# Optimization experiments

Measured on AMD Instinct MI355X. Metric: run time of the kernel, lower is better.

## Reference

```python
import jax, jax.numpy as jnp
import numpy as np

N, D = 8192, 128
TEMPERATURE = 0.5


def _l2_normalize(x, eps):
    # matches F.normalize / utils.sim_matrix norm clamping
    n = jnp.linalg.norm(x, axis=1, keepdims=True)
    return x / jnp.maximum(n, eps)


def setup_inputs() -> dict:
    key = jax.random.key(0)
    k1, k2, k3 = jax.random.split(key, 3)
    nodes = jax.random.normal(k1, (N, D), dtype=jnp.float32)
    pair_nodes = jax.random.normal(k2, (N, D), dtype=jnp.float32)
    nodes_labels = jax.random.randint(k3, (N,), 0, 20).astype(jnp.int64)
    # standard NT-Xent self-mask: exclude diagonal from the denominator
    mask = jnp.eye(N, dtype=bool)
    return {"nodes": nodes, "pair_nodes": pair_nodes,
            "nodes_labels": nodes_labels, "mask": mask}


def reference(nodes, pair_nodes, nodes_labels, mask):
    # z, z_p: F.normalize(..., dim=1), eps=1e-12
    z = _l2_normalize(nodes, 1e-12)
    z_p = _l2_normalize(pair_nodes, 1e-12)
    # pairwise cosine similarity [N, N] == z @ z_p.T since rows are unit-norm
    positive_similarity = jnp.einsum('id,jd->ij', z, z_p)
    nominator = jnp.exp(positive_similarity / TEMPERATURE)  # [N, N]
    # utils.sim_matrix(nodes, nodes): cosine sim matrix with eps=1e-8 clamp
    zn = _l2_normalize(nodes, 1e-8)
    similarity_matrix = jnp.einsum('id,jd->ij', zn, zn)  # [N, N]
    denominator = (~mask).astype(jnp.float32) * jnp.exp(similarity_matrix / TEMPERATURE)
    den_sum = jnp.sum(denominator, axis=1)  # [N]
    # torch broadcasting: [N,N] / [N] divides along the LAST axis (columns)
    loss_partial = -jnp.log(nominator / den_sum[None, :])
    loss = jnp.sum(loss_partial) / nodes.shape[0]
    return loss
```

## Files before the change

### kernel.cpp

```cpp
#include <hip/hip_runtime.h>

#define N 8192
#define D 128
#define NT 64
#define EXP_SCALE 2.8853900817779268f

typedef __bf16 bf16;
typedef __bf16 bf16x2 __attribute__((ext_vector_type(2)));
typedef __bf16 bf16x8 __attribute__((ext_vector_type(8)));
typedef float f32x4 __attribute__((ext_vector_type(4)));

#define ZBF_OFF 0
#define DEN_OFF (N * D * 2)
#define S_OFF   (DEN_OFF + N * 4)
#define SP_OFF  (S_OFF + 512)

__global__ __launch_bounds__(256) void norm_kernel(
    const float* __restrict__ nodes, const float* __restrict__ pair,
    bf16* __restrict__ zbf, float* __restrict__ svec, float* __restrict__ spvec)
{
    __shared__ float red[4][128];
    const int tid = threadIdx.x;
    const int lane = tid & 63, wave = tid >> 6;
    const bool isPair = blockIdx.x >= 128;
    const float* src = isPair ? pair : nodes;
    const int row0 = (blockIdx.x & 127) * 64 + wave * 16;

    float acc0 = 0.f, acc1 = 0.f;
    for (int rr = 0; rr < 16; ++rr) {
        const int row = row0 + rr;
        const float2 x = *(const float2*)(src + row * D + lane * 2);
        float ss = x.x * x.x + x.y * x.y;
        #pragma unroll
        for (int m = 32; m >= 1; m >>= 1) ss += __shfl_xor(ss, m, 64);
        const float nrm = sqrtf(ss);
        const float inv12 = 1.f / fmaxf(nrm, 1e-12f);
        acc0 += x.x * inv12;
        acc1 += x.y * inv12;
        if (!isPair) {
            const float inv8 = 1.f / fmaxf(nrm, 1e-8f);
            bf16x2 pk;
            pk[0] = (bf16)(x.x * inv8);
            pk[1] = (bf16)(x.y * inv8);
            *(bf16x2*)(zbf + row * D + lane * 2) = pk;
        }
    }
    red[wave][lane * 2]     = acc0;
    red[wave][lane * 2 + 1] = acc1;
    __syncthreads();
    if (tid < 128) {
        float* dst = isPair ? spvec : svec;
        atomicAdd(&dst[tid], red[0][tid] + red[1][tid] + red[2][tid] + red[3][tid]);
    }
}

#define LDP 80

__global__ __launch_bounds__(256) void gemm_kernel(
    const bf16* __restrict__ zbf, float* __restrict__ den)
{
    __shared__ bf16 As[128 * LDP];
    __shared__ bf16 Bs[128 * LDP];
    __shared__ float rowacc[128];
    __shared__ float colacc[128];

    int b = blockIdx.x;
    int ti = (int)((2.0 * NT + 1.0 - sqrt((2.0 * NT + 1.0) * (2.0 * NT + 1.0) - 8.0 * (double)b)) * 0.5);
    while (ti > 0 && ti * (2 * NT + 1 - ti) / 2 > b) --ti;
    while ((ti + 1) * (2 * NT - ti) / 2 <= b) ++ti;
    const int tj = ti + (b - ti * (2 * NT + 1 - ti) / 2);
    const bool diag = (ti == tj);

    const int tid  = threadIdx.x;
    const int lane = tid & 63, wave = tid >> 6;
    const int wm = wave >> 1, wn = wave & 1;
    const int quad = lane >> 4, c = lane & 15;
    const int ibase = ti * 128;
    const int jbase = tj * 128;

    if (tid < 128) { rowacc[tid] = 0.f; colacc[tid] = 0.f; }

    f32x4 acc[4][4];
    #pragma unroll
    for (int i = 0; i < 4; ++i)
        #pragma unroll
        for (int j = 0; j < 4; ++j) acc[i][j] = (f32x4){0.f, 0.f, 0.f, 0.f};

    #pragma unroll
    for (int kh = 0; kh < 2; ++kh) {
        __syncthreads();
        #pragma unroll
        for (int i = 0; i < 4; ++i) {
            const int chunk = tid + 256 * i;
            const int row = chunk >> 3;
            const int c8  = (chunk & 7) * 8;
            const uint4 va = *(const uint4*)(zbf + (ibase + row) * D + kh * 64 + c8);
            const uint4 vb = *(const uint4*)(zbf + (jbase + row) * D + kh * 64 + c8);
            *(uint4*)(&As[row * LDP + c8]) = va;
            *(uint4*)(&Bs[row * LDP + c8]) = vb;
        }
        __syncthreads();
        #pragma unroll
        for (int ks = 0; ks < 2; ++ks) {
            const int kk = ks * 32;
            bf16x8 af[4], bfr[4];
            #pragma unroll
            for (int mi = 0; mi < 4; ++mi)
                af[mi] = *(const bf16x8*)(&As[(wm * 64 + mi * 16 + c) * LDP + kk + quad * 8]);
            #pragma unroll
            for (int ni = 0; ni < 4; ++ni)
                bfr[ni] = *(const bf16x8*)(&Bs[(wn * 64 + ni * 16 + c) * LDP + kk + quad * 8]);
            #pragma unroll
            for (int mi = 0; mi < 4; ++mi)
                #pragma unroll
                for (int ni = 0; ni < 4; ++ni)
                    acc[mi][ni] = __builtin_amdgcn_mfma_f32_16x16x32_bf16(
                        af[mi], bfr[ni], acc[mi][ni], 0, 0, 0);
        }
    }

    float rowp[4][4];
    float colp[4];
    #pragma unroll
    for (int mi = 0; mi < 4; ++mi)
        #pragma unroll
        for (int r = 0; r < 4; ++r) rowp[mi][r] = 0.f;
    #pragma unroll
    for (int ni = 0; ni < 4; ++ni) colp[ni] = 0.f;

    #pragma unroll
    for (int mi = 0; mi < 4; ++mi) {
        const int lrow0 = wm * 64 + mi * 16 + quad * 4;
        #pragma unroll
        for (int ni = 0; ni < 4; ++ni) {
            const int lcol = wn * 64 + ni * 16 + c;
            const f32x4 cv = acc[mi][ni];
            #pragma unroll
            for (int r = 0; r < 4; ++r) {
                float e = __builtin_amdgcn_exp2f(cv[r] * EXP_SCALE);
                if (diag && (lrow0 + r == lcol)) e = 0.f;
                rowp[mi][r] += e;
                colp[ni]    += e;
            }
        }
    }

    #pragma unroll
    for (int mi = 0; mi < 4; ++mi)
        #pragma unroll
        for (int r = 0; r < 4; ++r) {
            #pragma unroll
            for (int m = 1; m <= 8; m <<= 1)
                rowp[mi][r] += __shfl_xor(rowp[mi][r], m, 64);
        }
    if (c == 0) {
        #pragma unroll
        for (int mi = 0; mi < 4; ++mi)
            #pragma unroll
            for (int r = 0; r < 4; ++r)
                atomicAdd(&rowacc[wm * 64 + mi * 16 + quad * 4 + r], rowp[mi][r]);
    }

    if (!diag) {
        #pragma unroll
        for (int ni = 0; ni < 4; ++ni) {
            colp[ni] += __shfl_xor(colp[ni], 16, 64);
            colp[ni] += __shfl_xor(colp[ni], 32, 64);
        }
        if (quad == 0) {
            #pragma unroll
            for (int ni = 0; ni < 4; ++ni)
                atomicAdd(&colacc[wn * 64 + ni * 16 + c], colp[ni]);
        }
    }

    __syncthreads();
    if (tid < 128) {
        atomicAdd(&den[ibase + tid], rowacc[tid]);
        if (!diag) atomicAdd(&den[jbase + tid], colacc[tid]);
    }
}

__global__ __launch_bounds__(256) void final_kernel(
    const float* __restrict__ den, const float* __restrict__ s,
    const float* __restrict__ sp, float* __restrict__ out)
{
    __shared__ float red[4];
    const int tid = threadIdx.x;
    float v = 0.f;
    for (int j = tid; j < N; j += 256) v += logf(den[j]);
    if (tid < 128) v -= s[tid] * sp[tid] * (1.f / 4096.f);
    #pragma unroll
    for (int m = 32; m >= 1; m >>= 1) v += __shfl_xor(v, m, 64);
    if ((tid & 63) == 0) red[tid >> 6] = v;
    __syncthreads();
    if (tid == 0) out[0] = red[0] + red[1] + red[2] + red[3];
}

extern "C" void kernel_launch(void* const* d_in, const int* in_sizes, int n_in,
                              void* d_out, int out_size, void* d_ws, size_t ws_size,
                              hipStream_t stream)
{
    const float* nodes = (const float*)d_in[0];
    const float* pair  = (const float*)d_in[1];

    char*  ws  = (char*)d_ws;
    bf16*  zbf = (bf16*)(ws + ZBF_OFF);
    float* den = (float*)(ws + DEN_OFF);
    float* s   = (float*)(ws + S_OFF);
    float* sp  = (float*)(ws + SP_OFF);

    hipMemsetAsync(ws + DEN_OFF, 0, N * 4 + 1024, stream);

    hipLaunchKernelGGL(norm_kernel, dim3(256), dim3(256), 0, stream,
                       nodes, pair, zbf, s, sp);
    hipLaunchKernelGGL(gemm_kernel, dim3(NT * (NT + 1) / 2), dim3(256), 0, stream,
                       zbf, den);
    hipLaunchKernelGGL(final_kernel, dim3(1), dim3(256), 0, stream,
                       den, s, sp, (float*)d_out);
}
```

Baseline: 352.8 us.

## Prescale normalized rows, widen norm kernel, prefetch second K-half into registers

The norm kernel now has 16 lanes handle each row with float4 loads, runs 1024 blocks, and writes the bf16 rows scaled by sqrt(2/ln2). This lets the GEMM epilogue call exp2 directly without a multiply. The GEMM kernel loads both K halves into registers up front and stores the second half to shared memory after the first half's MFMAs, so global-load latency overlaps compute. The prescaling shifts where bf16 rounding happens, so numerics change slightly, and holding the extra tile in registers raises register pressure.

Measured after the change: 361.7 us. +2.5%, slower.

```diff
diff --git a/kernel.cpp b/kernel.cpp
--- a/kernel.cpp
+++ b/kernel.cpp
@@ -3,10 +3,9 @@
 #define N 8192
 #define D 128
 #define NT 64
-#define EXP_SCALE 2.8853900817779268f
+#define PRESCALE 1.6986435984699773f
 
 typedef __bf16 bf16;
-typedef __bf16 bf16x2 __attribute__((ext_vector_type(2)));
 typedef __bf16 bf16x8 __attribute__((ext_vector_type(8)));
 typedef float f32x4 __attribute__((ext_vector_type(4)));
 
@@ -22,31 +21,42 @@
     __shared__ float red[4][128];
     const int tid = threadIdx.x;
     const int lane = tid & 63, wave = tid >> 6;
-    const bool isPair = blockIdx.x >= 128;
+    const int g = lane & 15, q = lane >> 4;
+    const bool isPair = blockIdx.x >= 512;
     const float* src = isPair ? pair : nodes;
-    const int row0 = (blockIdx.x & 127) * 64 + wave * 16;
-
-    float acc0 = 0.f, acc1 = 0.f;
-    for (int rr = 0; rr < 16; ++rr) {
-        const int row = row0 + rr;
-        const float2 x = *(const float2*)(src + row * D + lane * 2);
-        float ss = x.x * x.x + x.y * x.y;
-        #pragma unroll
-        for (int m = 32; m >= 1; m >>= 1) ss += __shfl_xor(ss, m, 64);
-        const float nrm = sqrtf(ss);
-        const float inv12 = 1.f / fmaxf(nrm, 1e-12f);
-        acc0 += x.x * inv12;
-        acc1 += x.y * inv12;
-        if (!isPair) {
-            const float inv8 = 1.f / fmaxf(nrm, 1e-8f);
-            bf16x2 pk;
-            pk[0] = (bf16)(x.x * inv8);
-            pk[1] = (bf16)(x.y * inv8);
-            *(bf16x2*)(zbf + row * D + lane * 2) = pk;
-        }
-    }
-    red[wave][lane * 2]     = acc0;
-    red[wave][lane * 2 + 1] = acc1;
+    const int row = (blockIdx.x & 511) * 16 + wave * 4 + q;
+
+    const float4 x0 = *(const float4*)(src + row * D + g * 8);
+    const float4 x1 = *(const float4*)(src + row * D + g * 8 + 4);
+    float ss = x0.x * x0.x + x0.y * x0.y + x0.z * x0.z + x0.w * x0.w
+             + x1.x * x1.x + x1.y * x1.y + x1.z * x1.z + x1.w * x1.w;
+    #pragma unroll
+    for (int m = 1; m <= 8; m <<= 1) ss += __shfl_xor(ss, m, 64);
+    const float nrm = sqrtf(ss);
+    const float inv12 = 1.f / fmaxf(nrm, 1e-12f);
+
+    float a[8] = { x0.x * inv12, x0.y * inv12, x0.z * inv12, x0.w * inv12,
+                   x1.x * inv12, x1.y * inv12, x1.z * inv12, x1.w * inv12 };
+
+    if (!isPair) {
+        const float sc = PRESCALE / fmaxf(nrm, 1e-8f);
+        bf16x8 pk;
+        pk[0] = (bf16)(x0.x * sc); pk[1] = (bf16)(x0.y * sc);
+        pk[2] = (bf16)(x0.z * sc); pk[3] = (bf16)(x0.w * sc);
+        pk[4] = (bf16)(x1.x * sc); pk[5] = (bf16)(x1.y * sc);
+        pk[6] = (bf16)(x1.z * sc); pk[7] = (bf16)(x1.w * sc);
+        *(bf16x8*)(zbf + row * D + g * 8) = pk;
+    }
+
+    #pragma unroll
+    for (int k = 0; k < 8; ++k) {
+        a[k] += __shfl_xor(a[k], 16, 64);
+        a[k] += __shfl_xor(a[k], 32, 64);
+    }
+    if (q == 0) {
+        #pragma unroll
+        for (int k = 0; k < 8; ++k) red[wave][g * 8 + k] = a[k];
+    }
     __syncthreads();
     if (tid < 128) {
         float* dst = isPair ? spvec : svec;
@@ -86,20 +96,32 @@
         #pragma unroll
         for (int j = 0; j < 4; ++j) acc[i][j] = (f32x4){0.f, 0.f, 0.f, 0.f};
 
+    uint4 va[4], vb[4];
+    #pragma unroll
+    for (int i = 0; i < 4; ++i) {
+        const int chunk = tid + 256 * i;
+        const int row = chunk >> 3, c8 = (chunk & 7) * 8;
+        va[i] = *(const uint4*)(zbf + (ibase + row) * D + c8);
+        vb[i] = *(const uint4*)(zbf + (jbase + row) * D + c8);
+    }
+    #pragma unroll
+    for (int i = 0; i < 4; ++i) {
+        const int chunk = tid + 256 * i;
+        const int row = chunk >> 3, c8 = (chunk & 7) * 8;
+        *(uint4*)(&As[row * LDP + c8]) = va[i];
+        *(uint4*)(&Bs[row * LDP + c8]) = vb[i];
+    }
+    #pragma unroll
+    for (int i = 0; i < 4; ++i) {
+        const int chunk = tid + 256 * i;
+        const int row = chunk >> 3, c8 = (chunk & 7) * 8;
+        va[i] = *(const uint4*)(zbf + (ibase + row) * D + 64 + c8);
+        vb[i] = *(const uint4*)(zbf + (jbase + row) * D + 64 + c8);
+    }
+    __syncthreads();
+
     #pragma unroll
     for (int kh = 0; kh < 2; ++kh) {
-        __syncthreads();
-        #pragma unroll
-        for (int i = 0; i < 4; ++i) {
-            const int chunk = tid + 256 * i;
-            const int row = chunk >> 3;
-            const int c8  = (chunk & 7) * 8;
-            const uint4 va = *(const uint4*)(zbf + (ibase + row) * D + kh * 64 + c8);
-            const uint4 vb = *(const uint4*)(zbf + (jbase + row) * D + kh * 64 + c8);
-            *(uint4*)(&As[row * LDP + c8]) = va;
-            *(uint4*)(&Bs[row * LDP + c8]) = vb;
-        }
-        __syncthreads();
         #pragma unroll
         for (int ks = 0; ks < 2; ++ks) {
             const int kk = ks * 32;
@@ -117,6 +139,17 @@
                     acc[mi][ni] = __builtin_amdgcn_mfma_f32_16x16x32_bf16(
                         af[mi], bfr[ni], acc[mi][ni], 0, 0, 0);
         }
+        if (kh == 0) {
+            __syncthreads();
+            #pragma unroll
+            for (int i = 0; i < 4; ++i) {
+                const int chunk = tid + 256 * i;
+                const int row = chunk >> 3, c8 = (chunk & 7) * 8;
+                *(uint4*)(&As[row * LDP + c8]) = va[i];
+                *(uint4*)(&Bs[row * LDP + c8]) = vb[i];
+            }
+            __syncthreads();
+        }
     }
 
     float rowp[4][4];
@@ -137,7 +170,7 @@
             const f32x4 cv = acc[mi][ni];
             #pragma unroll
             for (int r = 0; r < 4; ++r) {
-                float e = __builtin_amdgcn_exp2f(cv[r] * EXP_SCALE);
+                float e = __builtin_amdgcn_exp2f(cv[r]);
                 if (diag && (lrow0 + r == lcol)) e = 0.f;
                 rowp[mi][r] += e;
                 colp[ni]    += e;
@@ -212,7 +245,7 @@
 
     hipMemsetAsync(ws + DEN_OFF, 0, N * 4 + 1024, stream);
 
-    hipLaunchKernelGGL(norm_kernel, dim3(256), dim3(256), 0, stream,
+    hipLaunchKernelGGL(norm_kernel, dim3(1024), dim3(256), 0, stream,
                        nodes, pair, zbf, s, sp);
     hipLaunchKernelGGL(gemm_kernel, dim3(NT * (NT + 1) / 2), dim3(256), 0, stream,
                        zbf, den);
```
